# Kernel optimization log

Measured on AMD Instinct MI355X. Metric: run time of the kernel, lower is better.

The kernel has to match this reference:

```python
import jax, jax.numpy as jnp
import numpy as np

H = 1024
NH = 16
HD = H // NH  # 64

def setup_inputs() -> dict:
    key = jax.random.key(0)
    ks = jax.random.split(key, 6)
    scale = 0.02
    return {
        "hidden_states": jax.random.normal(ks[0], (2, 2048, H), dtype=jnp.float32),
        "Wq": jax.random.normal(ks[1], (H, H), dtype=jnp.float32) * scale,
        "bq": jnp.zeros((H,), dtype=jnp.float32),
        "Wk": jax.random.normal(ks[2], (H, H), dtype=jnp.float32) * scale,
        "bk": jnp.zeros((H,), dtype=jnp.float32),
        "Wv": jax.random.normal(ks[3], (H, H), dtype=jnp.float32) * scale,
        "bv": jnp.zeros((H,), dtype=jnp.float32),
        "Wo": jax.random.normal(ks[4], (H, H), dtype=jnp.float32) * scale,
        "bo": jnp.zeros((H,), dtype=jnp.float32),
    }

def _split_heads(x):
    # [B,S,H] -> [B,NH,S,HD]
    B, S, _ = x.shape
    return x.reshape(B, S, NH, HD).transpose(0, 2, 1, 3)

def reference(hidden_states, Wq, bq, Wk, bk, Wv, bv, Wo, bo):
    # Linear layers: y = x @ W^T + b (torch nn.Linear convention)
    q = _split_heads(hidden_states @ Wq.T + bq)
    k = _split_heads(hidden_states @ Wk.T + bk)
    v = _split_heads(hidden_states @ Wv.T + bv)
    scores = jnp.einsum("bhqd,bhkd->bhqk", q, k) / jnp.sqrt(jnp.float32(HD))
    probs = jax.nn.softmax(scores, axis=-1)  # dropout is identity in eval mode
    ctx = jnp.einsum("bhqk,bhkd->bhqd", probs, v)
    B, _, S, _ = ctx.shape
    ctx = ctx.transpose(0, 2, 1, 3).reshape(B, S, H)
    return ctx @ Wo.T + bo
```

## Files before the change

kernel.cpp:

```cpp
#include <hip/hip_runtime.h>
#include <hip/hip_bf16.h>

#define H_DIM 1024
#define NHEAD 16
#define HDIM  64
#define BATCH 2
#define SEQ   2048
#define MTOT  (BATCH*SEQ)
#define LOG2E 1.4426950408889634f

typedef _Float16 f16x8 __attribute__((ext_vector_type(8)));
typedef float  f32x4  __attribute__((ext_vector_type(4)));
typedef short  short8 __attribute__((ext_vector_type(8)));
typedef unsigned short u16;

static __device__ __forceinline__ u16 f2h(float f) {
  _Float16 h = (_Float16)f;
  return __builtin_bit_cast(u16, h);
}

static __device__ __forceinline__ void load_lds16(const void* g, void* l) {
  __builtin_amdgcn_global_load_lds(
      (const __attribute__((address_space(1))) unsigned int*)g,
      (__attribute__((address_space(3))) unsigned int*)l, 16, 0, 0);
}

#define N8X (MTOT * H_DIM / 8)
#define N8W (H_DIM * H_DIM / 8)

__global__ __launch_bounds__(256) void conv_all(
    const float* __restrict__ x,  const float* __restrict__ Wq,
    const float* __restrict__ Wk, const float* __restrict__ Wv,
    const float* __restrict__ Wo,
    u16* __restrict__ xb, u16* __restrict__ W3, u16* __restrict__ Wo16) {
  int gi = blockIdx.x * 256 + threadIdx.x;
  const float* src;
  u16* dst;
  int ci;
  if (gi < N8X) {
    src = x; dst = xb; ci = gi;
  } else {
    int j = gi - N8X;
    int which = j >> 17;
    ci = j & (N8W - 1);
    src = which == 0 ? Wq : (which == 1 ? Wk : (which == 2 ? Wv : Wo));
    dst = which < 3 ? W3 + (size_t)which * (N8W * 8) : Wo16;
  }
  float4 a = ((const float4*)src)[ci * 2];
  float4 b = ((const float4*)src)[ci * 2 + 1];
  union { u16 u[8]; short8 s; } r;
  r.u[0] = f2h(a.x); r.u[1] = f2h(a.y); r.u[2] = f2h(a.z); r.u[3] = f2h(a.w);
  r.u[4] = f2h(b.x); r.u[5] = f2h(b.y); r.u[6] = f2h(b.z); r.u[7] = f2h(b.w);
  *(short8*)&dst[ci * 8] = r.s;
}

#define BK 32

__global__ __launch_bounds__(256) void gemm_qkv(
    const u16* __restrict__ Xb, const u16* __restrict__ W3,
    const float* __restrict__ bq, const float* __restrict__ bk2,
    const float* __restrict__ bv,
    u16* __restrict__ qp, u16* __restrict__ kp, u16* __restrict__ vp) {
  __shared__ __align__(16) u16 Al[128 * BK];
  __shared__ __align__(16) u16 Bl[128 * BK];
  const int tid = threadIdx.x;
  const int w = tid >> 6, l = tid & 63, lg = l >> 4, lc = l & 15;
  const int wr = w >> 1, wc = w & 1;
  const int m0 = blockIdx.y * 128, n0 = blockIdx.x * 128;
  const int sr = w * 16 + (l >> 2);
  const int sc = (l & 3) * 8;

  f32x4 acc[4][4];
#pragma unroll
  for (int i = 0; i < 4; i++)
#pragma unroll
    for (int j = 0; j < 4; j++) acc[i][j] = (f32x4){0.f, 0.f, 0.f, 0.f};

  for (int k0 = 0; k0 < H_DIM; k0 += BK) {
    __syncthreads();
    load_lds16(&Xb[(size_t)(m0 + sr) * H_DIM + k0 + sc],      &Al[w * 512]);
    load_lds16(&Xb[(size_t)(m0 + 64 + sr) * H_DIM + k0 + sc], &Al[2048 + w * 512]);
    load_lds16(&W3[(size_t)(n0 + sr) * H_DIM + k0 + sc],      &Bl[w * 512]);
    load_lds16(&W3[(size_t)(n0 + 64 + sr) * H_DIM + k0 + sc], &Bl[2048 + w * 512]);
    __syncthreads();

    f16x8 af[4], bfr[4];
#pragma unroll
    for (int mi = 0; mi < 4; mi++)
      af[mi] = *(const f16x8*)&Al[(wr * 64 + mi * 16 + lc) * BK + lg * 8];
#pragma unroll
    for (int nj = 0; nj < 4; nj++)
      bfr[nj] = *(const f16x8*)&Bl[(wc * 64 + nj * 16 + lc) * BK + lg * 8];
#pragma unroll
    for (int mi = 0; mi < 4; mi++)
#pragma unroll
      for (int nj = 0; nj < 4; nj++)
        acc[mi][nj] = __builtin_amdgcn_mfma_f32_16x16x32_f16(af[mi], bfr[nj],
                                                             acc[mi][nj], 0, 0, 0);
  }

  const int np = n0 >> 10;
  u16* outp = np == 0 ? qp : (np == 1 ? kp : vp);
  const float* bias = np == 0 ? bq : (np == 1 ? bk2 : bv);
  const float scale = np == 0 ? (0.125f * LOG2E) : 1.0f;
  const int nc0 = (n0 & 1023) + wc * 64;
  float bvals[4];
#pragma unroll
  for (int nj = 0; nj < 4; nj++) bvals[nj] = bias[nc0 + nj * 16 + lc];
#pragma unroll
  for (int mi = 0; mi < 4; mi++)
#pragma unroll
    for (int nj = 0; nj < 4; nj++)
#pragma unroll
      for (int r = 0; r < 4; r++) {
        int row = m0 + wr * 64 + mi * 16 + lg * 4 + r;
        outp[(size_t)row * 1024 + nc0 + nj * 16 + lc] =
            f2h((acc[mi][nj][r] + bvals[nj]) * scale);
      }
}

__global__ __launch_bounds__(256) void gemm_oproj(
    const u16* __restrict__ A16, const u16* __restrict__ B16,
    const float* __restrict__ bias, float* __restrict__ out) {
  __shared__ __align__(16) u16 Al[128 * BK];
  __shared__ __align__(16) u16 Bl[128 * BK];
  const int tid = threadIdx.x;
  const int w = tid >> 6, l = tid & 63, lg = l >> 4, lc = l & 15;
  const int wr = w >> 1, wc = w & 1;
  const int m0 = blockIdx.y * 128, n0 = blockIdx.x * 128;
  const int sr = w * 16 + (l >> 2);
  const int sc = (l & 3) * 8;

  f32x4 acc[4][4];
#pragma unroll
  for (int i = 0; i < 4; i++)
#pragma unroll
    for (int j = 0; j < 4; j++) acc[i][j] = (f32x4){0.f, 0.f, 0.f, 0.f};

  for (int k0 = 0; k0 < H_DIM; k0 += BK) {
    __syncthreads();
    load_lds16(&A16[(size_t)(m0 + sr) * H_DIM + k0 + sc],      &Al[w * 512]);
    load_lds16(&A16[(size_t)(m0 + 64 + sr) * H_DIM + k0 + sc], &Al[2048 + w * 512]);
    load_lds16(&B16[(size_t)(n0 + sr) * H_DIM + k0 + sc],      &Bl[w * 512]);
    load_lds16(&B16[(size_t)(n0 + 64 + sr) * H_DIM + k0 + sc], &Bl[2048 + w * 512]);
    __syncthreads();

    f16x8 af[4], bfr[4];
#pragma unroll
    for (int mi = 0; mi < 4; mi++)
      af[mi] = *(const f16x8*)&Al[(wr * 64 + mi * 16 + lc) * BK + lg * 8];
#pragma unroll
    for (int nj = 0; nj < 4; nj++)
      bfr[nj] = *(const f16x8*)&Bl[(wc * 64 + nj * 16 + lc) * BK + lg * 8];
#pragma unroll
    for (int mi = 0; mi < 4; mi++)
#pragma unroll
      for (int nj = 0; nj < 4; nj++)
        acc[mi][nj] = __builtin_amdgcn_mfma_f32_16x16x32_f16(af[mi], bfr[nj],
                                                             acc[mi][nj], 0, 0, 0);
  }

  const int nc0 = n0 + wc * 64;
  float bvals[4];
#pragma unroll
  for (int nj = 0; nj < 4; nj++) bvals[nj] = bias[nc0 + nj * 16 + lc];
#pragma unroll
  for (int mi = 0; mi < 4; mi++)
#pragma unroll
    for (int nj = 0; nj < 4; nj++)
#pragma unroll
      for (int r = 0; r < 4; r++) {
        int row = m0 + wr * 64 + mi * 16 + lg * 4 + r;
        out[(size_t)row * 1024 + nc0 + nj * 16 + lc] = acc[mi][nj][r] + bvals[nj];
      }
}

#define KTILES 16

__global__ __launch_bounds__(512, 8) void attn_split(
    const u16* __restrict__ q, const u16* __restrict__ k,
    const u16* __restrict__ v, float* __restrict__ Opart,
    float* __restrict__ lpart) {
  __shared__ __align__(16) u16 Ks[64 * 64];
  __shared__ __align__(16) u16 Vt[64 * 64];
  __shared__ __align__(16) u16 Pws[8][16 * 64];

  const int tid = threadIdx.x;
  const int w = tid >> 6, l = tid & 63, lg = l >> 4, lc = l & 15;
  const int wg = (blockIdx.x & 7) * 128 + (blockIdx.x >> 3);
  const int qt   = wg & 15;
  const int half = (wg >> 4) & 1;
  const int h    = (wg >> 5) & 15;
  const int b    = wg >> 9;
  const size_t row0 = (size_t)b * SEQ;
  const int lc7 = lc & 7;

  f16x8 qf[2];
  {
    const u16* qp = q + (row0 + qt * 128 + w * 16 + lc) * H_DIM + h * HDIM + lg * 8;
    qf[0] = *(const f16x8*)(qp);
    qf[1] = *(const f16x8*)(qp + 32);
  }

  const int skey = tid >> 3, sd8 = tid & 7;
  const u16* ksrc = k + (row0 + half * 1024 + skey) * H_DIM + h * HDIM
                      + (sd8 ^ (skey & 7)) * 8;

  const int vd = tid & 63, ko = tid >> 6;
  const u16* vsrc = v + (row0 + half * 1024 + ko * 8) * H_DIM + h * HDIM + vd;
  const int vwo = vd * 64 + (ko ^ (vd & 7)) * 8;

  uint4 rV;
  {
    unsigned l0 = vsrc[0 * H_DIM], h0 = vsrc[1 * H_DIM];
    unsigned l1 = vsrc[2 * H_DIM], h1 = vsrc[3 * H_DIM];
    unsigned l2 = vsrc[4 * H_DIM], h2 = vsrc[5 * H_DIM];
    unsigned l3 = vsrc[6 * H_DIM], h3 = vsrc[7 * H_DIM];
    rV.x = l0 | (h0 << 16); rV.y = l1 | (h1 << 16);
    rV.z = l2 | (h2 << 16); rV.w = l3 | (h3 << 16);
  }

  f32x4 Oacc[4];
#pragma unroll
  for (int dj = 0; dj < 4; dj++) Oacc[dj] = (f32x4){0.f, 0.f, 0.f, 0.f};
  float lS = 0.f;

  for (int t = 0; t < KTILES; ++t) {
    __syncthreads();
    load_lds16(ksrc, &Ks[w * 512]);
    *(uint4*)&Vt[vwo] = rV;
    __syncthreads();
    ksrc += 64 * H_DIM;

    if (t + 1 < KTILES) {
      vsrc += 64 * H_DIM;
      unsigned l0 = vsrc[0 * H_DIM], h0 = vsrc[1 * H_DIM];
      unsigned l1 = vsrc[2 * H_DIM], h1 = vsrc[3 * H_DIM];
      unsigned l2 = vsrc[4 * H_DIM], h2 = vsrc[5 * H_DIM];
      unsigned l3 = vsrc[6 * H_DIM], h3 = vsrc[7 * H_DIM];
      rV.x = l0 | (h0 << 16); rV.y = l1 | (h1 << 16);
      rV.z = l2 | (h2 << 16); rV.w = l3 | (h3 << 16);
    }

    float ps = 0.f;
#pragma unroll
    for (int kj = 0; kj < 4; kj++) {
      f32x4 s = (f32x4){0.f, 0.f, 0.f, 0.f};
#pragma unroll
      for (int kt = 0; kt < 2; kt++) {
        f16x8 af = *(const f16x8*)&Ks[(kj * 16 + lc) * 64 + ((kt * 4 + lg) ^ lc7) * 8];
        s = __builtin_amdgcn_mfma_f32_16x16x32_f16(af, qf[kt], s, 0, 0, 0);
      }
      float e0 = exp2f(s[0]);
      float e1 = exp2f(s[1]);
      float e2 = exp2f(s[2]);
      float e3 = exp2f(s[3]);
      ps += (e0 + e1) + (e2 + e3);
      uint2 pw;
      pw.x = __builtin_bit_cast(unsigned, __builtin_amdgcn_cvt_pkrtz(e0, e1));
      pw.y = __builtin_bit_cast(unsigned, __builtin_amdgcn_cvt_pkrtz(e2, e3));
      *(uint2*)&Pws[w][lc * 64 + ((2 * kj + (lg >> 1)) ^ lc7) * 8 + (lg & 1) * 4] = pw;
    }
    lS += ps;

    f16x8 pb0 = *(const f16x8*)&Pws[w][lc * 64 + (lg ^ lc7) * 8];
    f16x8 pb1 = *(const f16x8*)&Pws[w][lc * 64 + ((4 + lg) ^ lc7) * 8];

#pragma unroll
    for (int dj = 0; dj < 4; dj++) {
      f16x8 vf0 = *(const f16x8*)&Vt[(dj * 16 + lc) * 64 + (lg ^ lc7) * 8];
      f16x8 vf1 = *(const f16x8*)&Vt[(dj * 16 + lc) * 64 + ((4 + lg) ^ lc7) * 8];
      Oacc[dj] = __builtin_amdgcn_mfma_f32_16x16x32_f16(vf0, pb0, Oacc[dj], 0, 0, 0);
      Oacc[dj] = __builtin_amdgcn_mfma_f32_16x16x32_f16(vf1, pb1, Oacc[dj], 0, 0, 0);
    }
  }

  lS += __shfl_xor(lS, 16);
  lS += __shfl_xor(lS, 32);
  const size_t grow = row0 + qt * 128 + w * 16 + lc;
  float* ob = Opart + ((size_t)half * MTOT + grow) * H_DIM + h * HDIM + lg * 4;
#pragma unroll
  for (int dj = 0; dj < 4; dj++) {
    f32x4 o = Oacc[dj];
    *(float4*)(ob + dj * 16) = (float4){o[0], o[1], o[2], o[3]};
  }
  if (lg == 0)
    lpart[((size_t)half * NHEAD + h) * MTOT + grow] = lS;
}

__global__ __launch_bounds__(256) void combine_kernel(
    const float* __restrict__ Opart, const float* __restrict__ lpart,
    u16* __restrict__ ctx) {
  int gi = blockIdx.x * 256 + threadIdx.x;
  int r  = gi >> 7;
  int d0 = (gi & 127) * 8;
  int hh = d0 >> 6;
  float lt = lpart[(size_t)hh * MTOT + r] + lpart[(size_t)(NHEAD + hh) * MTOT + r];
  float inv = 1.f / lt;
  const float* o0 = Opart + (size_t)r * H_DIM + d0;
  const float* o1 = o0 + (size_t)MTOT * H_DIM;
  float4 a = *(const float4*)o0, b = *(const float4*)(o0 + 4);
  float4 c = *(const float4*)o1, d = *(const float4*)(o1 + 4);
  union { u16 u[8]; short8 s; } rr;
  rr.u[0] = f2h((a.x + c.x) * inv); rr.u[1] = f2h((a.y + c.y) * inv);
  rr.u[2] = f2h((a.z + c.z) * inv); rr.u[3] = f2h((a.w + c.w) * inv);
  rr.u[4] = f2h((b.x + d.x) * inv); rr.u[5] = f2h((b.y + d.y) * inv);
  rr.u[6] = f2h((b.z + d.z) * inv); rr.u[7] = f2h((b.w + d.w) * inv);
  *(short8*)&ctx[(size_t)gi * 8] = rr.s;
}

extern "C" void kernel_launch(void* const* d_in, const int* in_sizes, int n_in,
                              void* d_out, int out_size, void* d_ws, size_t ws_size,
                              hipStream_t stream) {
  const float* x  = (const float*)d_in[0];
  const float* Wq = (const float*)d_in[1];
  const float* bq = (const float*)d_in[2];
  const float* Wk = (const float*)d_in[3];
  const float* bk = (const float*)d_in[4];
  const float* Wv = (const float*)d_in[5];
  const float* bv = (const float*)d_in[6];
  const float* Wo = (const float*)d_in[7];
  const float* bo = (const float*)d_in[8];
  float* out = (float*)d_out;

  const size_t PL = (size_t)MTOT * H_DIM;
  const size_t WN = (size_t)H_DIM * H_DIM;
  u16* xb    = (u16*)d_ws;
  u16* W3    = xb + PL;
  u16* qp    = W3 + 3 * WN;
  u16* kp    = qp + PL;
  u16* vp    = kp + PL;
  u16* ctxp  = vp + PL;
  u16* Wo16  = ctxp + PL;
  float* Opart = (float*)(Wo16 + WN);
  float* lpart = Opart + 2 * PL;

  conv_all<<<(N8X + 4 * N8W) / 256, 256, 0, stream>>>(
      x, Wq, Wk, Wv, Wo, xb, W3, Wo16);

  gemm_qkv<<<dim3(3072 / 128, MTOT / 128), 256, 0, stream>>>(
      xb, W3, bq, bk, bv, qp, kp, vp);

  attn_split<<<dim3(1024), 512, 0, stream>>>(qp, kp, vp, Opart, lpart);

  combine_kernel<<<dim3((MTOT * H_DIM / 8) / 256), 256, 0, stream>>>(
      Opart, lpart, ctxp);

  gemm_oproj<<<dim3(1024 / 128, MTOT / 128), 256, 0, stream>>>(
      ctxp, Wo16, bo, out);
}
```

Measured before the change: 143.1 us.

## Use 32x32 MFMA in attention with register-resident P via permlane32 swap

The split-K attention kernel moves from 16x16x32 to 32x32x16 MFMA tiles, with 4 waves of 32 query rows each instead of 8 waves of 16. The softmax numerators stay in registers and are rearranged into the B-operand layout with permlane32_swap, which removes the per-wave P staging buffer in LDS. The partial outputs are also stored as fp16 instead of fp32, which halves the Opart traffic between attention and combine at some cost in precision. Fewer threads per block and larger accumulators raise register pressure per thread.

```diff
diff --git a/kernel.cpp b/kernel.cpp
--- a/kernel.cpp
+++ b/kernel.cpp
@@ -11,7 +11,9 @@
 
 typedef _Float16 f16x8 __attribute__((ext_vector_type(8)));
 typedef float  f32x4  __attribute__((ext_vector_type(4)));
+typedef float  f32x16 __attribute__((ext_vector_type(16)));
 typedef short  short8 __attribute__((ext_vector_type(8)));
+typedef unsigned uint2v __attribute__((ext_vector_type(2)));
 typedef unsigned short u16;
 
 static __device__ __forceinline__ u16 f2h(float f) {
@@ -177,119 +179,162 @@
 
 #define KTILES 16
 
-__global__ __launch_bounds__(512, 8) void attn_split(
+__global__ __launch_bounds__(256, 4) void attn_mfma7(
     const u16* __restrict__ q, const u16* __restrict__ k,
-    const u16* __restrict__ v, float* __restrict__ Opart,
+    const u16* __restrict__ v, u16* __restrict__ Opart,
     float* __restrict__ lpart) {
   __shared__ __align__(16) u16 Ks[64 * 64];
   __shared__ __align__(16) u16 Vt[64 * 64];
-  __shared__ __align__(16) u16 Pws[8][16 * 64];
 
   const int tid = threadIdx.x;
-  const int w = tid >> 6, l = tid & 63, lg = l >> 4, lc = l & 15;
+  const int w = tid >> 6, l = tid & 63;
+  const int l31 = l & 31, l5 = l >> 5;
   const int wg = (blockIdx.x & 7) * 128 + (blockIdx.x >> 3);
   const int qt   = wg & 15;
   const int half = (wg >> 4) & 1;
   const int h    = (wg >> 5) & 15;
   const int b    = wg >> 9;
   const size_t row0 = (size_t)b * SEQ;
-  const int lc7 = lc & 7;
-
-  f16x8 qf[2];
+  const int grow = qt * 128 + w * 32 + l31;
+
+  f16x8 qf[4];
   {
-    const u16* qp = q + (row0 + qt * 128 + w * 16 + lc) * H_DIM + h * HDIM + lg * 8;
-    qf[0] = *(const f16x8*)(qp);
-    qf[1] = *(const f16x8*)(qp + 32);
-  }
-
-  const int skey = tid >> 3, sd8 = tid & 7;
-  const u16* ksrc = k + (row0 + half * 1024 + skey) * H_DIM + h * HDIM
-                      + (sd8 ^ (skey & 7)) * 8;
+    const u16* qp = q + (row0 + grow) * H_DIM + h * HDIM + 8 * l5;
+#pragma unroll
+    for (int dc = 0; dc < 4; dc++)
+      qf[dc] = *(const f16x8*)(qp + dc * 16);
+  }
+
+  const int c1 = tid + 256;
+  const u16* ksrc0 = k + (row0 + half * 1024 + (tid >> 3)) * H_DIM + h * HDIM
+                       + ((tid & 7) ^ ((tid >> 3) & 7)) * 8;
+  const u16* ksrc1 = k + (row0 + half * 1024 + (c1 >> 3)) * H_DIM + h * HDIM
+                       + ((c1 & 7) ^ ((c1 >> 3) & 7)) * 8;
 
   const int vd = tid & 63, ko = tid >> 6;
   const u16* vsrc = v + (row0 + half * 1024 + ko * 8) * H_DIM + h * HDIM + vd;
-  const int vwo = vd * 64 + (ko ^ (vd & 7)) * 8;
-
-  uint4 rV;
+  const int vwo0 = vd * 64 + ((ko)     ^ (vd & 7)) * 8;
+  const int vwo1 = vd * 64 + ((ko + 4) ^ (vd & 7)) * 8;
+
+  uint4 rV0, rV1;
   {
-    unsigned l0 = vsrc[0 * H_DIM], h0 = vsrc[1 * H_DIM];
-    unsigned l1 = vsrc[2 * H_DIM], h1 = vsrc[3 * H_DIM];
-    unsigned l2 = vsrc[4 * H_DIM], h2 = vsrc[5 * H_DIM];
-    unsigned l3 = vsrc[6 * H_DIM], h3 = vsrc[7 * H_DIM];
-    rV.x = l0 | (h0 << 16); rV.y = l1 | (h1 << 16);
-    rV.z = l2 | (h2 << 16); rV.w = l3 | (h3 << 16);
-  }
-
-  f32x4 Oacc[4];
-#pragma unroll
-  for (int dj = 0; dj < 4; dj++) Oacc[dj] = (f32x4){0.f, 0.f, 0.f, 0.f};
+    unsigned a0 = vsrc[0 * H_DIM], a1 = vsrc[1 * H_DIM];
+    unsigned a2 = vsrc[2 * H_DIM], a3 = vsrc[3 * H_DIM];
+    unsigned a4 = vsrc[4 * H_DIM], a5 = vsrc[5 * H_DIM];
+    unsigned a6 = vsrc[6 * H_DIM], a7 = vsrc[7 * H_DIM];
+    rV0.x = a0 | (a1 << 16); rV0.y = a2 | (a3 << 16);
+    rV0.z = a4 | (a5 << 16); rV0.w = a6 | (a7 << 16);
+    const u16* v2 = vsrc + 32 * H_DIM;
+    unsigned b0 = v2[0 * H_DIM], b1 = v2[1 * H_DIM];
+    unsigned b2 = v2[2 * H_DIM], b3 = v2[3 * H_DIM];
+    unsigned b4 = v2[4 * H_DIM], b5 = v2[5 * H_DIM];
+    unsigned b6 = v2[6 * H_DIM], b7 = v2[7 * H_DIM];
+    rV1.x = b0 | (b1 << 16); rV1.y = b2 | (b3 << 16);
+    rV1.z = b4 | (b5 << 16); rV1.w = b6 | (b7 << 16);
+  }
+
+  f32x16 Oacc[2];
+#pragma unroll
+  for (int i = 0; i < 2; i++)
+#pragma unroll
+    for (int r = 0; r < 16; r++) Oacc[i][r] = 0.f;
   float lS = 0.f;
 
   for (int t = 0; t < KTILES; ++t) {
     __syncthreads();
-    load_lds16(ksrc, &Ks[w * 512]);
-    *(uint4*)&Vt[vwo] = rV;
-    __syncthreads();
-    ksrc += 64 * H_DIM;
+    load_lds16(ksrc0, &Ks[w * 512]);
+    load_lds16(ksrc1, &Ks[2048 + w * 512]);
+    *(uint4*)&Vt[vwo0] = rV0;
+    *(uint4*)&Vt[vwo1] = rV1;
+    __syncthreads();
+    ksrc0 += 64 * H_DIM;
+    ksrc1 += 64 * H_DIM;
 
     if (t + 1 < KTILES) {
       vsrc += 64 * H_DIM;
-      unsigned l0 = vsrc[0 * H_DIM], h0 = vsrc[1 * H_DIM];
-      unsigned l1 = vsrc[2 * H_DIM], h1 = vsrc[3 * H_DIM];
-      unsigned l2 = vsrc[4 * H_DIM], h2 = vsrc[5 * H_DIM];
-      unsigned l3 = vsrc[6 * H_DIM], h3 = vsrc[7 * H_DIM];
-      rV.x = l0 | (h0 << 16); rV.y = l1 | (h1 << 16);
-      rV.z = l2 | (h2 << 16); rV.w = l3 | (h3 << 16);
+      unsigned a0 = vsrc[0 * H_DIM], a1 = vsrc[1 * H_DIM];
+      unsigned a2 = vsrc[2 * H_DIM], a3 = vsrc[3 * H_DIM];
+      unsigned a4 = vsrc[4 * H_DIM], a5 = vsrc[5 * H_DIM];
+      unsigned a6 = vsrc[6 * H_DIM], a7 = vsrc[7 * H_DIM];
+      rV0.x = a0 | (a1 << 16); rV0.y = a2 | (a3 << 16);
+      rV0.z = a4 | (a5 << 16); rV0.w = a6 | (a7 << 16);
+      const u16* v2 = vsrc + 32 * H_DIM;
+      unsigned b0 = v2[0 * H_DIM], b1 = v2[1 * H_DIM];
+      unsigned b2 = v2[2 * H_DIM], b3 = v2[3 * H_DIM];
+      unsigned b4 = v2[4 * H_DIM], b5 = v2[5 * H_DIM];
+      unsigned b6 = v2[6 * H_DIM], b7 = v2[7 * H_DIM];
+      rV1.x = b0 | (b1 << 16); rV1.y = b2 | (b3 << 16);
+      rV1.z = b4 | (b5 << 16); rV1.w = b6 | (b7 << 16);
     }
 
+    unsigned pw[2][4][2];
     float ps = 0.f;
 #pragma unroll
-    for (int kj = 0; kj < 4; kj++) {
-      f32x4 s = (f32x4){0.f, 0.f, 0.f, 0.f};
-#pragma unroll
-      for (int kt = 0; kt < 2; kt++) {
-        f16x8 af = *(const f16x8*)&Ks[(kj * 16 + lc) * 64 + ((kt * 4 + lg) ^ lc7) * 8];
-        s = __builtin_amdgcn_mfma_f32_16x16x32_f16(af, qf[kt], s, 0, 0, 0);
-      }
-      float e0 = exp2f(s[0]);
-      float e1 = exp2f(s[1]);
-      float e2 = exp2f(s[2]);
-      float e3 = exp2f(s[3]);
-      ps += (e0 + e1) + (e2 + e3);
-      uint2 pw;
-      pw.x = __builtin_bit_cast(unsigned, __builtin_amdgcn_cvt_pkrtz(e0, e1));
-      pw.y = __builtin_bit_cast(unsigned, __builtin_amdgcn_cvt_pkrtz(e2, e3));
-      *(uint2*)&Pws[w][lc * 64 + ((2 * kj + (lg >> 1)) ^ lc7) * 8 + (lg & 1) * 4] = pw;
+    for (int kc = 0; kc < 2; kc++) {
+      f32x16 s;
+#pragma unroll
+      for (int r = 0; r < 16; r++) s[r] = 0.f;
+      const int key = kc * 32 + l31;
+      const int rowb = key * 64, keyx = key & 7;
+#pragma unroll
+      for (int dc = 0; dc < 4; dc++) {
+        f16x8 af = *(const f16x8*)&Ks[rowb + (((dc << 1) + l5) ^ keyx) * 8];
+        s = __builtin_amdgcn_mfma_f32_32x32x16_f16(af, qf[dc], s, 0, 0, 0);
+      }
+#pragma unroll
+      for (int rh = 0; rh < 4; rh++)
+#pragma unroll
+        for (int k1 = 0; k1 < 2; k1++) {
+          float e0 = exp2f(s[4 * rh + 2 * k1]);
+          float e1 = exp2f(s[4 * rh + 2 * k1 + 1]);
+          ps += e0 + e1;
+          pw[kc][rh][k1] = __builtin_bit_cast(
+              unsigned, __builtin_amdgcn_cvt_pkrtz(e0, e1));
+        }
     }
     lS += ps;
 
-    f16x8 pb0 = *(const f16x8*)&Pws[w][lc * 64 + (lg ^ lc7) * 8];
-    f16x8 pb1 = *(const f16x8*)&Pws[w][lc * 64 + ((4 + lg) ^ lc7) * 8];
-
-#pragma unroll
-    for (int dj = 0; dj < 4; dj++) {
-      f16x8 vf0 = *(const f16x8*)&Vt[(dj * 16 + lc) * 64 + (lg ^ lc7) * 8];
-      f16x8 vf1 = *(const f16x8*)&Vt[(dj * 16 + lc) * 64 + ((4 + lg) ^ lc7) * 8];
-      Oacc[dj] = __builtin_amdgcn_mfma_f32_16x16x32_f16(vf0, pb0, Oacc[dj], 0, 0, 0);
-      Oacc[dj] = __builtin_amdgcn_mfma_f32_16x16x32_f16(vf1, pb1, Oacc[dj], 0, 0, 0);
+#pragma unroll
+    for (int kcc = 0; kcc < 4; kcc++) {
+      union { unsigned u[4]; f16x8 v8; } bf;
+      const int kcs = kcc >> 1, rhA = (kcc & 1) << 1;
+#pragma unroll
+      for (int k1 = 0; k1 < 2; k1++) {
+        uint2v xy = __builtin_amdgcn_permlane32_swap(
+            pw[kcs][rhA][k1], pw[kcs][rhA + 1][k1], false, false);
+        bf.u[k1] = xy.x;
+        bf.u[2 + k1] = xy.y;
+      }
+#pragma unroll
+      for (int dc2 = 0; dc2 < 2; dc2++) {
+        const int d = dc2 * 32 + l31;
+        f16x8 vf = *(const f16x8*)&Vt[d * 64 + (((kcc << 1) + l5) ^ (d & 7)) * 8];
+        Oacc[dc2] = __builtin_amdgcn_mfma_f32_32x32x16_f16(vf, bf.v8,
+                                                           Oacc[dc2], 0, 0, 0);
+      }
     }
   }
 
-  lS += __shfl_xor(lS, 16);
   lS += __shfl_xor(lS, 32);
-  const size_t grow = row0 + qt * 128 + w * 16 + lc;
-  float* ob = Opart + ((size_t)half * MTOT + grow) * H_DIM + h * HDIM + lg * 4;
-#pragma unroll
-  for (int dj = 0; dj < 4; dj++) {
-    f32x4 o = Oacc[dj];
-    *(float4*)(ob + dj * 16) = (float4){o[0], o[1], o[2], o[3]};
-  }
-  if (lg == 0)
-    lpart[((size_t)half * NHEAD + h) * MTOT + grow] = lS;
+  u16* ob = Opart + ((size_t)half * MTOT + row0 + grow) * H_DIM + h * HDIM;
+#pragma unroll
+  for (int dc2 = 0; dc2 < 2; dc2++)
+#pragma unroll
+    for (int rh = 0; rh < 4; rh++) {
+      int d0 = dc2 * 32 + 8 * rh + 4 * l5;
+      uint2 pd;
+      pd.x = __builtin_bit_cast(unsigned, __builtin_amdgcn_cvt_pkrtz(
+          Oacc[dc2][4 * rh + 0], Oacc[dc2][4 * rh + 1]));
+      pd.y = __builtin_bit_cast(unsigned, __builtin_amdgcn_cvt_pkrtz(
+          Oacc[dc2][4 * rh + 2], Oacc[dc2][4 * rh + 3]));
+      *(uint2*)&ob[d0] = pd;
+    }
+  if (l < 32)
+    lpart[((size_t)half * NHEAD + h) * MTOT + row0 + grow] = lS;
 }
 
 __global__ __launch_bounds__(256) void combine_kernel(
-    const float* __restrict__ Opart, const float* __restrict__ lpart,
+    const u16* __restrict__ Opart, const float* __restrict__ lpart,
     u16* __restrict__ ctx) {
   int gi = blockIdx.x * 256 + threadIdx.x;
   int r  = gi >> 7;
@@ -297,15 +342,15 @@
   int hh = d0 >> 6;
   float lt = lpart[(size_t)hh * MTOT + r] + lpart[(size_t)(NHEAD + hh) * MTOT + r];
   float inv = 1.f / lt;
-  const float* o0 = Opart + (size_t)r * H_DIM + d0;
-  const float* o1 = o0 + (size_t)MTOT * H_DIM;
-  float4 a = *(const float4*)o0, b = *(const float4*)(o0 + 4);
-  float4 c = *(const float4*)o1, d = *(const float4*)(o1 + 4);
+  short8 a = *(const short8*)&Opart[(size_t)r * H_DIM + d0];
+  short8 c = *(const short8*)&Opart[(size_t)MTOT * H_DIM + (size_t)r * H_DIM + d0];
   union { u16 u[8]; short8 s; } rr;
-  rr.u[0] = f2h((a.x + c.x) * inv); rr.u[1] = f2h((a.y + c.y) * inv);
-  rr.u[2] = f2h((a.z + c.z) * inv); rr.u[3] = f2h((a.w + c.w) * inv);
-  rr.u[4] = f2h((b.x + d.x) * inv); rr.u[5] = f2h((b.y + d.y) * inv);
-  rr.u[6] = f2h((b.z + d.z) * inv); rr.u[7] = f2h((b.w + d.w) * inv);
+#pragma unroll
+  for (int j = 0; j < 8; j++) {
+    float fa = (float)__builtin_bit_cast(_Float16, (u16)a[j]);
+    float fc = (float)__builtin_bit_cast(_Float16, (u16)c[j]);
+    rr.u[j] = f2h((fa + fc) * inv);
+  }
   *(short8*)&ctx[(size_t)gi * 8] = rr.s;
 }
 
@@ -332,8 +377,8 @@
   u16* vp    = kp + PL;
   u16* ctxp  = vp + PL;
   u16* Wo16  = ctxp + PL;
-  float* Opart = (float*)(Wo16 + WN);
-  float* lpart = Opart + 2 * PL;
+  u16* Opart = Wo16 + WN;
+  float* lpart = (float*)(Opart + 2 * PL);
 
   conv_all<<<(N8X + 4 * N8W) / 256, 256, 0, stream>>>(
       x, Wq, Wk, Wv, Wo, xb, W3, Wo16);
@@ -341,7 +386,7 @@
   gemm_qkv<<<dim3(3072 / 128, MTOT / 128), 256, 0, stream>>>(
       xb, W3, bq, bk, bv, qp, kp, vp);
 
-  attn_split<<<dim3(1024), 512, 0, stream>>>(qp, kp, vp, Opart, lpart);
+  attn_mfma7<<<dim3(1024), 256, 0, stream>>>(qp, kp, vp, Opart, lpart);
 
   combine_kernel<<<dim3((MTOT * H_DIM / 8) / 256), 256, 0, stream>>>(
       Opart, lpart, ctxp);
```

Measured after the change: 137.4 us, median of 2. 4.0% less time.
